# Kernel tuning notes

Measured on AMD Instinct MI355X. Metric: run time of the kernel, lower is better.

Reference implementation:

```python
import jax, jax.numpy as jnp
import numpy as np

N = 100_000      # nodes
E = 1_600_000    # edges (avg degree 16)
IN, H, OUT = 128, 64, 32
G = 128          # graphs in batch
EPS = 1e-5


def setup_inputs() -> dict:
    key = jax.random.key(0)
    ks = jax.random.split(key, 12)
    x = jax.random.normal(ks[0], (N, IN), jnp.float32)
    edge_index = jax.random.randint(ks[1], (2, E), 0, N, dtype=jnp.int32)
    batch = jnp.sort(jax.random.randint(ks[2], (N,), 0, G, dtype=jnp.int32))
    # GCNConv weights (glorot-ish scaling), shared BatchNorm params, final linear
    W1 = jax.random.normal(ks[3], (IN, H), jnp.float32) / np.sqrt(IN)
    b1 = jnp.zeros((H,), jnp.float32)
    W2 = jax.random.normal(ks[4], (H, H), jnp.float32) / np.sqrt(H)
    b2 = jnp.zeros((H,), jnp.float32)
    gamma = jnp.ones((H,), jnp.float32)
    beta = jnp.zeros((H,), jnp.float32)
    linW = jax.random.normal(ks[5], (H, OUT), jnp.float32) / np.sqrt(H)
    linb = jnp.zeros((OUT,), jnp.float32)
    return dict(x=x, edge_index=edge_index, batch=batch, W1=W1, b1=b1,
                W2=W2, b2=b2, gamma=gamma, beta=beta, linW=linW, linb=linb)


def _gcn_edges(edge_index):
    # add self loops (PyG GCNConv default) and symmetric normalization
    loop = jnp.arange(N, dtype=edge_index.dtype)
    src = jnp.concatenate([edge_index[0], loop])
    dst = jnp.concatenate([edge_index[1], loop])
    deg = jax.ops.segment_sum(jnp.ones_like(src, jnp.float32), dst, num_segments=N)
    dis = jnp.where(deg > 0, jax.lax.rsqrt(deg), 0.0)
    norm = dis[src] * dis[dst]          # [E+N]
    return src, dst, norm


def _gcn_conv(h, W, b, src, dst, norm):
    h = h @ W                            # [N, out] small GEMM first (PyG order)
    msg = h[src] * norm[:, None]         # gather + edgewise normalize
    return jax.ops.segment_sum(msg, dst, num_segments=N) + b  # scatter-add


def _batchnorm(h, gamma, beta):
    # training-mode batch stats over nodes (biased variance, as torch BN)
    mean = h.mean(axis=0)
    var = jnp.mean((h - mean) ** 2, axis=0)
    return (h - mean) * jax.lax.rsqrt(var + EPS) * gamma + beta


def reference(x, edge_index, batch, W1, b1, W2, b2, gamma, beta, linW, linb):
    src, dst, norm = _gcn_edges(edge_index)
    h = jax.nn.relu(_batchnorm(_gcn_conv(x, W1, b1, src, dst, norm), gamma, beta))
    h = jax.nn.relu(_batchnorm(_gcn_conv(h, W2, b2, src, dst, norm), gamma, beta))
    # global mean pool over graph ids
    sums = jax.ops.segment_sum(h, batch, num_segments=G)
    cnts = jax.ops.segment_sum(jnp.ones((N,), h.dtype), batch, num_segments=G)
    pooled = sums / jnp.maximum(cnts, 1.0)[:, None]   # [G, H]
    return pooled @ linW + linb                        # [G, OUT]
```

## Files before the change

kernel.cpp:

```cpp
#include <hip/hip_runtime.h>

#define NNODES 100000
#define NEDGES 1600000
#define FIN 128
#define FH 64
#define FOUT 32
#define NGRAPH 128
#define EPSV 1e-5f

#define SCAN_BT 256
#define NBLK ((NNODES + SCAN_BT - 1) / SCAN_BT)
#define GM ((NNODES + 63) / 64)
#define FILLBLK 2048

typedef unsigned short ushort_t;
typedef __attribute__((ext_vector_type(8))) short bf16x8;
typedef __attribute__((ext_vector_type(4))) float f32x4;

__device__ inline unsigned f2bf(float f) {
  union { float f; unsigned u; } x;
  x.f = f;
  return (x.u + 0x7fffu + ((x.u >> 16) & 1u)) >> 16;
}
__device__ inline float bflo(unsigned u) {
  union { unsigned u; float f; } x;
  x.u = u << 16;
  return x.f;
}
__device__ inline float bfhi(unsigned u) {
  union { unsigned u; float f; } x;
  x.u = u & 0xffff0000u;
  return x.f;
}


__global__ void k_deg_accum(const int* __restrict__ dst, int* __restrict__ deg) {
  const int SLICE = NNODES / 8;
  int xcd = blockIdx.x & 7;
  int lo = xcd * SLICE, hi = lo + SLICE;
  int chunk = blockIdx.x >> 3;
  int nchunk = gridDim.x >> 3;
  for (int i = chunk * blockDim.x + threadIdx.x; i < NEDGES; i += nchunk * blockDim.x) {
    int d = dst[i];
    if (d >= lo && d < hi) atomicAdd(&deg[d], 1);
  }
}


__global__ void k_blocksum(const int* __restrict__ deg, int* __restrict__ bsum) {
  __shared__ int ls[SCAN_BT];
  int b = blockIdx.x, t = threadIdx.x;
  int i = b * SCAN_BT + t;
  ls[t] = (i < NNODES) ? deg[i] : 0;
  __syncthreads();
  for (int s = SCAN_BT / 2; s > 0; s >>= 1) {
    if (t < s) ls[t] += ls[t + s];
    __syncthreads();
  }
  if (t == 0) bsum[b] = ls[0];
}

__global__ void k_scan_bsums(const int* __restrict__ bsum, int* __restrict__ boff) {
  __shared__ int ls[512];
  int t = threadIdx.x;
  int v = (t < NBLK) ? bsum[t] : 0;
  ls[t] = v;
  __syncthreads();
  for (int s = 1; s < 512; s <<= 1) {
    int add = (t >= s) ? ls[t - s] : 0;
    __syncthreads();
    ls[t] += add;
    __syncthreads();
  }
  if (t < NBLK) boff[t] = ls[t] - v;
}

__global__ void k_scan_final(const int* __restrict__ deg, const int* __restrict__ boff,
                             int* __restrict__ off, float* __restrict__ dis) {
  __shared__ int ls[SCAN_BT];
  int b = blockIdx.x, t = threadIdx.x;
  int i = b * SCAN_BT + t;
  int v = (i < NNODES) ? deg[i] : 0;
  ls[t] = v;
  __syncthreads();
  for (int s = 1; s < SCAN_BT; s <<= 1) {
    int add = (t >= s) ? ls[t - s] : 0;
    __syncthreads();
    ls[t] += add;
    __syncthreads();
  }
  if (i < NNODES) {
    off[i] = boff[b] + ls[t] - v;
    dis[i] = rsqrtf((float)v + 1.0f);
  }
  if (i == NNODES - 1) off[NNODES] = boff[b] + ls[t];
}


template <int K, bool BN>
__device__ __forceinline__ void gemm_body(int bid, const float* __restrict__ A,
                                          const float* __restrict__ W,
                                          const float* __restrict__ stats,
                                          const float* __restrict__ gamma,
                                          const float* __restrict__ beta,
                                          const float* __restrict__ dis,
                                          ushort_t* __restrict__ out) {
  const int WT = K + 8;
  __shared__ ushort_t wt[64 * (K + 8)];
  __shared__ float bn_sc[K], bn_sh[K];
  if (BN && threadIdx.x < K) {
    int f = threadIdx.x;
    float mean = stats[f] * (1.0f / NNODES);
    float var = stats[K + f] * (1.0f / NNODES) - mean * mean;
    float s = gamma[f] * rsqrtf(var + EPSV);
    bn_sc[f] = s;
    bn_sh[f] = beta[f] - mean * s;
  }
  for (int idx = threadIdx.x; idx < K * 64; idx += 256) {
    int k = idx >> 6, col = idx & 63;
    wt[col * WT + k] = (ushort_t)f2bf(W[idx]);
  }
  __syncthreads();

  int wave = threadIdx.x >> 6;
  int lane = threadIdx.x & 63;
  int rrow = lane & 15;
  int g = lane >> 4;
  int row0 = (bid * 4 + wave) * 16;
  int arow = min(row0 + rrow, NNODES - 1);
  const float* a = A + (long long)arow * K;

  f32x4 acc0 = {0.f, 0.f, 0.f, 0.f}, acc1 = acc0, acc2 = acc0, acc3 = acc0;

#pragma unroll
  for (int ks = 0; ks < K / 32; ++ks) {
    int koff = ks * 32 + g * 8;
    float4 xa = *(const float4*)(a + koff);
    float4 xb = *(const float4*)(a + koff + 4);
    float xs[8] = {xa.x, xa.y, xa.z, xa.w, xb.x, xb.y, xb.z, xb.w};
    if (BN) {
#pragma unroll
      for (int j = 0; j < 8; ++j)
        xs[j] = fmaxf(fmaf(xs[j], bn_sc[koff + j], bn_sh[koff + j]), 0.0f);
    }
    bf16x8 af;
#pragma unroll
    for (int j = 0; j < 8; ++j) af[j] = (short)f2bf(xs[j]);
    bf16x8 b0 = *(const bf16x8*)&wt[(0 * 16 + rrow) * WT + koff];
    bf16x8 b1 = *(const bf16x8*)&wt[(1 * 16 + rrow) * WT + koff];
    bf16x8 b2 = *(const bf16x8*)&wt[(2 * 16 + rrow) * WT + koff];
    bf16x8 b3 = *(const bf16x8*)&wt[(3 * 16 + rrow) * WT + koff];
    acc0 = __builtin_amdgcn_mfma_f32_16x16x32_bf16(af, b0, acc0, 0, 0, 0);
    acc1 = __builtin_amdgcn_mfma_f32_16x16x32_bf16(af, b1, acc1, 0, 0, 0);
    acc2 = __builtin_amdgcn_mfma_f32_16x16x32_bf16(af, b2, acc2, 0, 0, 0);
    acc3 = __builtin_amdgcn_mfma_f32_16x16x32_bf16(af, b3, acc3, 0, 0, 0);
  }

  int orow0 = row0 + g * 4;
#pragma unroll
  for (int r = 0; r < 4; ++r) {
    int orow = orow0 + r;
    if (orow < NNODES) {
      float d = dis[orow];
      ushort_t* o = out + (long long)orow * FH + rrow;
      o[0] = (ushort_t)f2bf(acc0[r] * d);
      o[16] = (ushort_t)f2bf(acc1[r] * d);
      o[32] = (ushort_t)f2bf(acc2[r] * d);
      o[48] = (ushort_t)f2bf(acc3[r] * d);
    }
  }
}

template <int K, bool BN>
__global__ void k_gemm_mfma(const float* __restrict__ A, const float* __restrict__ W,
                            const float* __restrict__ stats, const float* __restrict__ gamma,
                            const float* __restrict__ beta, const float* __restrict__ dis,
                            ushort_t* __restrict__ out) {
  gemm_body<K, BN>(blockIdx.x, A, W, stats, gamma, beta, dis, out);
}


__global__ void k_fill_gemm1(const float* __restrict__ x, const float* __restrict__ W1,
                             const float* __restrict__ dis, ushort_t* __restrict__ bufA,
                             const int* __restrict__ src, const int* __restrict__ dst,
                             const int* __restrict__ off, int* __restrict__ cursor,
                             int* __restrict__ csr) {
  if (blockIdx.x < GM) {
    gemm_body<FIN, false>(blockIdx.x, x, W1, nullptr, nullptr, nullptr, dis, bufA);
  } else {
    int bb = blockIdx.x - GM;
    const int SLICE = NNODES / 8;
    int xcd = bb & 7;
    int lo = xcd * SLICE, hi = lo + SLICE;
    int chunk = bb >> 3;
    int nchunk = FILLBLK >> 3;
    for (int i = chunk * blockDim.x + threadIdx.x; i < NEDGES; i += nchunk * blockDim.x) {
      int d = dst[i];
      if (d >= lo && d < hi) {
        int p = atomicAdd(&cursor[d], 1);
        csr[off[d] + p] = src[i];
      }
    }
  }
}


#define ACC8(acc, u, ok)                       \
  acc[0] += (ok) ? bflo(u.x) : 0.0f;           \
  acc[1] += (ok) ? bfhi(u.x) : 0.0f;           \
  acc[2] += (ok) ? bflo(u.y) : 0.0f;           \
  acc[3] += (ok) ? bfhi(u.y) : 0.0f;           \
  acc[4] += (ok) ? bflo(u.z) : 0.0f;           \
  acc[5] += (ok) ? bfhi(u.z) : 0.0f;           \
  acc[6] += (ok) ? bflo(u.w) : 0.0f;           \
  acc[7] += (ok) ? bfhi(u.w) : 0.0f;

__global__ void k_gather(const ushort_t* __restrict__ hs, const int* __restrict__ csr,
                         const int* __restrict__ off, const float* __restrict__ dis,
                         float* __restrict__ out, float* __restrict__ stats) {
  __shared__ float ls[2 * FH];
  int tid = threadIdx.x;
  if (tid < 2 * FH) ls[tid] = 0.0f;
  __syncthreads();
  int lane = tid & 63;
  int q = lane >> 3;
  int i = lane & 7;
  int wid = (blockIdx.x * blockDim.x + tid) >> 6;
  int nw = (gridDim.x * blockDim.x) >> 6;
  const int HALF = NNODES / 2;
  float s1[8], s2[8];
#pragma unroll
  for (int f = 0; f < 8; ++f) s1[f] = s2[f] = 0.0f;

  for (int p = wid; p < HALF; p += nw) {
    int dA = p, dB = p + HALF;
    int bA = off[dA], eA = off[dA + 1];
    int bB = off[dB], eB = off[dB + 1];
    uint4 selfA = *(const uint4*)(hs + (long long)dA * FH + i * 8);
    uint4 selfB = *(const uint4*)(hs + (long long)dB * FH + i * 8);
    float accA[8], accB[8];
    bool q0 = (q == 0);
    ACC8(((float(&)[8])accA), selfA, q0);
#pragma unroll
    for (int f = 0; f < 8; ++f) accA[f] = q0 ? accA[f] : 0.0f;
#pragma unroll
    for (int f = 0; f < 8; ++f) accA[f] = 0.0f;
#pragma unroll
    for (int f = 0; f < 8; ++f) accB[f] = 0.0f;
    ACC8(accA, selfA, q0);
    ACC8(accB, selfB, q0);

    int nA = (eA - bA + 15) >> 4, nB = (eB - bB + 15) >> 4;
    int niter = max(nA, nB);
    int lastA = max(eA - 1, 0), lastB = max(eB - 1, 0);
    int kA0 = bA + q, kA1 = bA + q + 8;
    int kB0 = bB + q, kB1 = bB + q + 8;
    for (int j = 0; j < niter; ++j) {
      int a0 = kA0 + 16 * j, a1 = kA1 + 16 * j;
      int b0 = kB0 + 16 * j, b1 = kB1 + 16 * j;
      int cA0 = csr[min(a0, lastA)];
      int cA1 = csr[min(a1, lastA)];
      int cB0 = csr[min(b0, lastB)];
      int cB1 = csr[min(b1, lastB)];
      uint4 uA0 = *(const uint4*)(hs + (long long)cA0 * FH + i * 8);
      uint4 uA1 = *(const uint4*)(hs + (long long)cA1 * FH + i * 8);
      uint4 uB0 = *(const uint4*)(hs + (long long)cB0 * FH + i * 8);
      uint4 uB1 = *(const uint4*)(hs + (long long)cB1 * FH + i * 8);
      bool A0 = a0 < eA, A1 = a1 < eA, B0 = b0 < eB, B1 = b1 < eB;
      ACC8(accA, uA0, A0);
      ACC8(accA, uA1, A1);
      ACC8(accB, uB0, B0);
      ACC8(accB, uB1, B1);
    }
#pragma unroll
    for (int f = 0; f < 8; ++f) {
      accA[f] += __shfl_xor(accA[f], 8);
      accA[f] += __shfl_xor(accA[f], 16);
      accA[f] += __shfl_xor(accA[f], 32);
      accB[f] += __shfl_xor(accB[f], 8);
      accB[f] += __shfl_xor(accB[f], 16);
      accB[f] += __shfl_xor(accB[f], 32);
    }
    float ddA = dis[dA], ddB = dis[dB];
#pragma unroll
    for (int f = 0; f < 8; ++f) {
      accA[f] *= ddA;
      accB[f] *= ddB;
      s1[f] += accA[f] + accB[f];
      s2[f] += accA[f] * accA[f] + accB[f] * accB[f];
    }
    if (q == 0) {
      float4 v0 = {accA[0], accA[1], accA[2], accA[3]};
      float4 v1 = {accA[4], accA[5], accA[6], accA[7]};
      *(float4*)(out + (long long)dA * FH + i * 8) = v0;
      *(float4*)(out + (long long)dA * FH + i * 8 + 4) = v1;
    } else if (q == 1) {
      float4 v0 = {accB[0], accB[1], accB[2], accB[3]};
      float4 v1 = {accB[4], accB[5], accB[6], accB[7]};
      *(float4*)(out + (long long)dB * FH + i * 8) = v0;
      *(float4*)(out + (long long)dB * FH + i * 8 + 4) = v1;
    }
  }
  if (q == 2) {
#pragma unroll
    for (int f = 0; f < 8; ++f) {
      atomicAdd(&ls[i * 8 + f], s1[f]);
      atomicAdd(&ls[FH + i * 8 + f], s2[f]);
    }
  }
  __syncthreads();
  if (tid < 2 * FH) atomicAdd(&stats[tid], ls[tid]);
}


#define POOL_WAVES 1024

__global__ void k_pool(const float* __restrict__ h, const int* __restrict__ batch,
                       const float* __restrict__ stats, const float* __restrict__ gamma,
                       const float* __restrict__ beta, float* __restrict__ pooled,
                       float* __restrict__ cnt) {
  const int CHUNK = (NNODES + POOL_WAVES - 1) / POOL_WAVES;
  int lane = threadIdx.x & 63;
  int wid = (blockIdx.x * blockDim.x + threadIdx.x) >> 6;
  int start = wid * CHUNK;
  if (start >= NNODES) return;
  int end = min(start + CHUNK, NNODES);
  float mean = stats[lane] * (1.0f / NNODES);
  float var = stats[FH + lane] * (1.0f / NNODES) - mean * mean;
  float sc = gamma[lane] * rsqrtf(var + EPSV);
  float sh = beta[lane] - mean * sc;
  int cur = batch[start];
  float acc = 0.0f;
  int cl = 0;
  for (int n = start; n < end; ++n) {
    int g = batch[n];
    if (g != cur) {
      atomicAdd(&pooled[cur * FH + lane], acc);
      if (lane == 0) atomicAdd(&cnt[cur], (float)cl);
      acc = 0.0f;
      cl = 0;
      cur = g;
    }
    float v = fmaf(h[(long long)n * FH + lane], sc, sh);
    acc += fmaxf(v, 0.0f);
    ++cl;
  }
  atomicAdd(&pooled[cur * FH + lane], acc);
  if (lane == 0) atomicAdd(&cnt[cur], (float)cl);
}


__global__ void k_final(const float* __restrict__ pooled, const float* __restrict__ cnt,
                        const float* __restrict__ linW, const float* __restrict__ linb,
                        float* __restrict__ out) {
  int t = blockIdx.x * blockDim.x + threadIdx.x;
  if (t >= NGRAPH * FOUT) return;
  int g = t / FOUT, o = t % FOUT;
  float inv = 1.0f / fmaxf(cnt[g], 1.0f);
  float acc = linb[o];
#pragma unroll
  for (int k = 0; k < FH; ++k) acc = fmaf(pooled[g * FH + k] * inv, linW[k * FOUT + o], acc);
  out[t] = acc;
}

extern "C" void kernel_launch(void* const* d_in, const int* in_sizes, int n_in,
                              void* d_out, int out_size, void* d_ws, size_t ws_size,
                              hipStream_t stream) {
  const float* x = (const float*)d_in[0];
  const int* edge_index = (const int*)d_in[1];
  const int* batch = (const int*)d_in[2];
  const float* W1 = (const float*)d_in[3];
  const float* W2 = (const float*)d_in[5];
  const float* gamma = (const float*)d_in[7];
  const float* beta = (const float*)d_in[8];
  const float* linW = (const float*)d_in[9];
  const float* linb = (const float*)d_in[10];
  float* out = (float*)d_out;

  const int* esrc = edge_index;
  const int* edst = edge_index + NEDGES;

  ushort_t* bufA = (ushort_t*)d_ws;
  float* bufB = (float*)d_ws + (long long)NNODES * FH;
  float* dis = bufB + (long long)NNODES * FH;
  int* off = (int*)(dis + NNODES);
  int* csr = off + (NNODES + 1);
  int* bsum = csr + NEDGES;
  int* boff = bsum + NBLK;
  int* deg = boff + NBLK;
  int* cursor = deg + NNODES;
  float* stats1 = (float*)(cursor + NNODES);
  float* stats2 = stats1 + 2 * FH;
  float* pooled = stats2 + 2 * FH;
  float* cnt = pooled + NGRAPH * FH;

  const int BT = 256;

  hipMemsetAsync(deg, 0,
                 (size_t)(2 * NNODES + 2 * 2 * FH + NGRAPH * FH + NGRAPH) * sizeof(int), stream);

  k_deg_accum<<<2048, BT, 0, stream>>>(edst, deg);
  k_blocksum<<<NBLK, SCAN_BT, 0, stream>>>(deg, bsum);
  k_scan_bsums<<<1, 512, 0, stream>>>(bsum, boff);
  k_scan_final<<<NBLK, SCAN_BT, 0, stream>>>(deg, boff, off, dis);
  k_fill_gemm1<<<GM + FILLBLK, BT, 0, stream>>>(x, W1, dis, bufA, esrc, edst, off, cursor, csr);

  k_gather<<<2048, BT, 0, stream>>>(bufA, csr, off, dis, bufB, stats1);

  k_gemm_mfma<FH, true><<<GM, BT, 0, stream>>>(bufB, W2, stats1, gamma, beta, dis, bufA);
  k_gather<<<2048, BT, 0, stream>>>(bufA, csr, off, dis, bufB, stats2);

  k_pool<<<POOL_WAVES * 64 / BT, BT, 0, stream>>>(bufB, batch, stats2, gamma, beta, pooled, cnt);
  k_final<<<(NGRAPH * FOUT + BT - 1) / BT, BT, 0, stream>>>(pooled, cnt, linW, linb, out);
}
```

Baseline: 419.9 us.

## Split gather feature dimension across block classes, one node per wave

The gather kernel now splits the 64 features into two 32-feature halves handled by separate block classes. Each wave processes one destination node, with 16 lanes covering edges and 4 lanes covering features, instead of two nodes with 8 edge lanes each. The grid is doubled to keep the same node coverage per class. The GEMM A-loads and the gather output stores are made nontemporal to reduce cache pollution. Gathering half-rows (64 bytes) may improve L2 locality per class, but it doubles the reads of csr and offsets and the number of per-row transactions.

```diff
diff --git a/kernel.cpp b/kernel.cpp
--- a/kernel.cpp
+++ b/kernel.cpp
@@ -12,6 +12,7 @@
 #define NBLK ((NNODES + SCAN_BT - 1) / SCAN_BT)
 #define GM ((NNODES + 63) / 64)
 #define FILLBLK 2048
+#define GATHER_BLK 4096
 
 typedef unsigned short ushort_t;
 typedef __attribute__((ext_vector_type(8))) short bf16x8;
@@ -135,8 +136,8 @@
 #pragma unroll
   for (int ks = 0; ks < K / 32; ++ks) {
     int koff = ks * 32 + g * 8;
-    float4 xa = *(const float4*)(a + koff);
-    float4 xb = *(const float4*)(a + koff + 4);
+    f32x4 xa = __builtin_nontemporal_load((const f32x4*)(a + koff));
+    f32x4 xb = __builtin_nontemporal_load((const f32x4*)(a + koff + 4));
     float xs[8] = {xa.x, xa.y, xa.z, xa.w, xb.x, xb.y, xb.z, xb.w};
     if (BN) {
 #pragma unroll
@@ -223,89 +224,65 @@
   if (tid < 2 * FH) ls[tid] = 0.0f;
   __syncthreads();
   int lane = tid & 63;
-  int q = lane >> 3;
-  int i = lane & 7;
-  int wid = (blockIdx.x * blockDim.x + tid) >> 6;
-  int nw = (gridDim.x * blockDim.x) >> 6;
-  const int HALF = NNODES / 2;
+  int q = lane >> 2;
+  int i = lane & 3;
+  int cls = (blockIdx.x >> 2) & 1;
+  int blk_in_cls = ((blockIdx.x >> 3) << 2) | (blockIdx.x & 3);
+  int wid = blk_in_cls * 4 + (tid >> 6);
+  const int NW = (GATHER_BLK / 2) * 4;
+  int fbase = cls * 32 + i * 8;
   float s1[8], s2[8];
 #pragma unroll
   for (int f = 0; f < 8; ++f) s1[f] = s2[f] = 0.0f;
 
-  for (int p = wid; p < HALF; p += nw) {
-    int dA = p, dB = p + HALF;
-    int bA = off[dA], eA = off[dA + 1];
-    int bB = off[dB], eB = off[dB + 1];
-    uint4 selfA = *(const uint4*)(hs + (long long)dA * FH + i * 8);
-    uint4 selfB = *(const uint4*)(hs + (long long)dB * FH + i * 8);
-    float accA[8], accB[8];
+  for (int d = wid; d < NNODES; d += NW) {
+    int b = off[d], e = off[d + 1];
+    uint4 self = *(const uint4*)(hs + (long long)d * FH + fbase);
+    float acc[8];
+#pragma unroll
+    for (int f = 0; f < 8; ++f) acc[f] = 0.0f;
     bool q0 = (q == 0);
-    ACC8(((float(&)[8])accA), selfA, q0);
-#pragma unroll
-    for (int f = 0; f < 8; ++f) accA[f] = q0 ? accA[f] : 0.0f;
-#pragma unroll
-    for (int f = 0; f < 8; ++f) accA[f] = 0.0f;
-#pragma unroll
-    for (int f = 0; f < 8; ++f) accB[f] = 0.0f;
-    ACC8(accA, selfA, q0);
-    ACC8(accB, selfB, q0);
-
-    int nA = (eA - bA + 15) >> 4, nB = (eB - bB + 15) >> 4;
-    int niter = max(nA, nB);
-    int lastA = max(eA - 1, 0), lastB = max(eB - 1, 0);
-    int kA0 = bA + q, kA1 = bA + q + 8;
-    int kB0 = bB + q, kB1 = bB + q + 8;
+    ACC8(acc, self, q0);
+    int deg = e - b;
+    int niter = (deg + 31) >> 5;
+    int last = max(e - 1, 0);
     for (int j = 0; j < niter; ++j) {
-      int a0 = kA0 + 16 * j, a1 = kA1 + 16 * j;
-      int b0 = kB0 + 16 * j, b1 = kB1 + 16 * j;
-      int cA0 = csr[min(a0, lastA)];
-      int cA1 = csr[min(a1, lastA)];
-      int cB0 = csr[min(b0, lastB)];
-      int cB1 = csr[min(b1, lastB)];
-      uint4 uA0 = *(const uint4*)(hs + (long long)cA0 * FH + i * 8);
-      uint4 uA1 = *(const uint4*)(hs + (long long)cA1 * FH + i * 8);
-      uint4 uB0 = *(const uint4*)(hs + (long long)cB0 * FH + i * 8);
-      uint4 uB1 = *(const uint4*)(hs + (long long)cB1 * FH + i * 8);
-      bool A0 = a0 < eA, A1 = a1 < eA, B0 = b0 < eB, B1 = b1 < eB;
-      ACC8(accA, uA0, A0);
-      ACC8(accA, uA1, A1);
-      ACC8(accB, uB0, B0);
-      ACC8(accB, uB1, B1);
+      int a0 = b + q + 32 * j;
+      int a1 = a0 + 16;
+      int c0 = csr[min(a0, last)];
+      int c1 = csr[min(a1, last)];
+      uint4 u0 = *(const uint4*)(hs + (long long)c0 * FH + fbase);
+      uint4 u1 = *(const uint4*)(hs + (long long)c1 * FH + fbase);
+      bool ok0 = a0 < e, ok1 = a1 < e;
+      ACC8(acc, u0, ok0);
+      ACC8(acc, u1, ok1);
     }
 #pragma unroll
     for (int f = 0; f < 8; ++f) {
-      accA[f] += __shfl_xor(accA[f], 8);
-      accA[f] += __shfl_xor(accA[f], 16);
-      accA[f] += __shfl_xor(accA[f], 32);
-      accB[f] += __shfl_xor(accB[f], 8);
-      accB[f] += __shfl_xor(accB[f], 16);
-      accB[f] += __shfl_xor(accB[f], 32);
-    }
-    float ddA = dis[dA], ddB = dis[dB];
+      acc[f] += __shfl_xor(acc[f], 4);
+      acc[f] += __shfl_xor(acc[f], 8);
+      acc[f] += __shfl_xor(acc[f], 16);
+      acc[f] += __shfl_xor(acc[f], 32);
+    }
+    float dd = dis[d];
 #pragma unroll
     for (int f = 0; f < 8; ++f) {
-      accA[f] *= ddA;
-      accB[f] *= ddB;
-      s1[f] += accA[f] + accB[f];
-      s2[f] += accA[f] * accA[f] + accB[f] * accB[f];
+      acc[f] *= dd;
+      s1[f] += acc[f];
+      s2[f] += acc[f] * acc[f];
     }
     if (q == 0) {
-      float4 v0 = {accA[0], accA[1], accA[2], accA[3]};
-      float4 v1 = {accA[4], accA[5], accA[6], accA[7]};
-      *(float4*)(out + (long long)dA * FH + i * 8) = v0;
-      *(float4*)(out + (long long)dA * FH + i * 8 + 4) = v1;
-    } else if (q == 1) {
-      float4 v0 = {accB[0], accB[1], accB[2], accB[3]};
-      float4 v1 = {accB[4], accB[5], accB[6], accB[7]};
-      *(float4*)(out + (long long)dB * FH + i * 8) = v0;
-      *(float4*)(out + (long long)dB * FH + i * 8 + 4) = v1;
-    }
-  }
-  if (q == 2) {
+      f32x4 v0 = {acc[0], acc[1], acc[2], acc[3]};
+      f32x4 v1 = {acc[4], acc[5], acc[6], acc[7]};
+      __builtin_nontemporal_store(v0, (f32x4*)(out + (long long)d * FH + fbase));
+      __builtin_nontemporal_store(v1, (f32x4*)(out + (long long)d * FH + fbase + 4));
+    }
+  }
+  if (q == 1) {
 #pragma unroll
     for (int f = 0; f < 8; ++f) {
-      atomicAdd(&ls[i * 8 + f], s1[f]);
-      atomicAdd(&ls[FH + i * 8 + f], s2[f]);
+      atomicAdd(&ls[fbase + f], s1[f]);
+      atomicAdd(&ls[FH + fbase + f], s2[f]);
     }
   }
   __syncthreads();
@@ -405,10 +382,10 @@
   k_scan_final<<<NBLK, SCAN_BT, 0, stream>>>(deg, boff, off, dis);
   k_fill_gemm1<<<GM + FILLBLK, BT, 0, stream>>>(x, W1, dis, bufA, esrc, edst, off, cursor, csr);
 
-  k_gather<<<2048, BT, 0, stream>>>(bufA, csr, off, dis, bufB, stats1);
+  k_gather<<<GATHER_BLK, BT, 0, stream>>>(bufA, csr, off, dis, bufB, stats1);
 
   k_gemm_mfma<FH, true><<<GM, BT, 0, stream>>>(bufB, W2, stats1, gamma, beta, dis, bufA);
-  k_gather<<<2048, BT, 0, stream>>>(bufA, csr, off, dis, bufB, stats2);
+  k_gather<<<GATHER_BLK, BT, 0, stream>>>(bufA, csr, off, dis, bufB, stats2);
 
   k_pool<<<POOL_WAVES * 64 / BT, BT, 0, stream>>>(bufB, batch, stats2, gamma, beta, pooled, cnt);
   k_final<<<(NGRAPH * FOUT + BT - 1) / BT, BT, 0, stream>>>(pooled, cnt, linW, linb, out);
```

Measured after the change: 583.3 us. 1.39x slower.
